# Kernel optimization log

Hardware: AMD Instinct MI355X
Metric: run time of the kernel (lower is better)

The kernel has to match this reference:

```python
import jax, jax.numpy as jnp
import numpy as np

KERNEL_SIZE = 4
SCALE = 0.5


def setup_inputs() -> dict:
    key = jax.random.key(0)
    k1, k2, k3 = jax.random.split(key, 3)
    M, K, N = 16384, 1024, 4096
    x = jax.random.normal(k1, (M, K), dtype=jnp.float32)
    weight = jax.random.normal(k2, (N, K), dtype=jnp.float32)
    bias = jax.random.normal(k3, (N,), dtype=jnp.float32)
    return {"x": x, "weight": weight, "bias": bias}


def reference(x, weight, bias):
    # y = x @ W^T + b : (M, N)
    y = jnp.einsum('mk,nk->mn', x, weight) + bias[None, :]
    M, N = y.shape
    valid_n = (N // KERNEL_SIZE) * KERNEL_SIZE
    # MaxPool1d(kernel_size, stride=kernel_size): (M, N//k, k) -> max over window
    pooled = jnp.max(y[:, :valid_n].reshape(M, valid_n // KERNEL_SIZE, KERNEL_SIZE), axis=-1)
    # sum over pooled features, then scale -> (M,)
    return jnp.sum(pooled, axis=-1) * SCALE
```

## Files before the change

### kernel.cpp

```cpp
#include <hip/hip_runtime.h>
#include <stdint.h>

#define M_DIM 16384
#define K_DIM 1024
#define N_DIM 4096
#define BM 128
#define BN 128
#define LDSP 40

#define TILE_ELEMS (128 * K_DIM)
#define SLAB_ELEMS (128 * 32)
#define NSLAB_X ((M_DIM / 128) * 32)
#define NSLAB_W ((N_DIM / 128) * 32)
#define CROW 20

typedef __bf16 bf16;
typedef __attribute__((ext_vector_type(8))) __bf16 bf16x8;
typedef __attribute__((ext_vector_type(4))) float f32x4;

__device__ __forceinline__ uint32_t pack2_bf16(float a, float b) {
    uint32_t ua = __float_as_uint(a);
    uint32_t ub = __float_as_uint(b);
    ua += 0x7fffu + ((ua >> 16) & 1u);
    ub += 0x7fffu + ((ub >> 16) & 1u);
    return (ua >> 16) | (ub & 0xffff0000u);
}

__global__ __launch_bounds__(256) void convert_pack_kernel(
    const float* __restrict__ x, const float* __restrict__ w,
    bf16* __restrict__ xp, bf16* __restrict__ wp, float* __restrict__ out)
{
    int slab = blockIdx.x;
    const int t = threadIdx.x;
    if (slab < (M_DIM / 256)) out[slab * 256 + t] = 0.f;

    const float* src;
    bf16* dst;
    if (slab < NSLAB_X) { src = x; dst = xp; }
    else                { slab -= NSLAB_X; src = w; dst = wp; }
    const int tile = slab >> 5;
    const int s    = slab & 31;

    __shared__ uint32_t ls[128 * CROW];

    {
        const int r  = t >> 1;
        const int kh = (t & 1) * 16;
        const float4* p = (const float4*)(src + (size_t)(tile * 128 + r) * K_DIM + s * 32 + kh);
        float4 a = p[0], b = p[1], c = p[2], d = p[3];
        uint4* lp = (uint4*)&ls[r * CROW + (t & 1) * 8];
        uint4 v0, v1;
        v0.x = pack2_bf16(a.x, a.y); v0.y = pack2_bf16(a.z, a.w);
        v0.z = pack2_bf16(b.x, b.y); v0.w = pack2_bf16(b.z, b.w);
        v1.x = pack2_bf16(c.x, c.y); v1.y = pack2_bf16(c.z, c.w);
        v1.z = pack2_bf16(d.x, d.y); v1.w = pack2_bf16(d.z, d.w);
        lp[0] = v0; lp[1] = v1;
    }
    __syncthreads();
    uint4* dst4 = (uint4*)(dst + (size_t)tile * TILE_ELEMS + (size_t)s * SLAB_ELEMS);
    #pragma unroll
    for (int p = 0; p < 2; ++p) {
        const int c    = t + p * 256;
        const int lane = c & 63;
        const int rb   = c >> 6;
        const int q    = lane >> 4;
        const int lrow = lane & 15;
        const int r    = rb * 16 + lrow;
        const uint4* lp = (const uint4*)&ls[r * CROW + q * 4];
        dst4[c] = lp[0];
    }
}

__device__ __forceinline__ void load_set(const bf16* base, uint32_t off, bf16x8* f) {
    #pragma unroll
    for (int i = 0; i < 4; ++i) f[i] = *(const bf16x8*)(base + off + i * 512);
}

__device__ __forceinline__ void do_mfma(const bf16x8* af, const bf16x8* bf,
                                        f32x4 acc[4][4]) {
    #pragma unroll
    for (int i = 0; i < 4; ++i)
        #pragma unroll
        for (int j = 0; j < 4; ++j)
            acc[i][j] = __builtin_amdgcn_mfma_f32_16x16x32_bf16(af[i], bf[j], acc[i][j], 0, 0, 0);
}

__global__ __launch_bounds__(256, 4) void gemm_pool_direct_kernel(
    const bf16* __restrict__ xp, const bf16* __restrict__ wp,
    const float* __restrict__ bias, float* __restrict__ out)
{
    const int b     = blockIdx.x;
    const int xcd   = b & 7;
    const int o     = (b >> 3) & 7;
    const int bx    = (b >> 6) & 31;
    const int phase = b >> 11;
    const int by    = phase * 64 + xcd * 8 + o;

    const int lane = threadIdx.x & 63;
    const int wave = threadIdx.x >> 6;
    const int wm = wave >> 1;
    const int wn = wave & 1;
    const int lr = lane & 15;
    const int quad = lane >> 4;

    const bf16* Ab = xp + (size_t)by * TILE_ELEMS;
    const bf16* Bb = wp + (size_t)bx * TILE_ELEMS;
    const uint32_t aoff = (wm * 4) * 512 + lane * 8;
    const uint32_t boff = (wn * 4) * 512 + lane * 8;

    f32x4 acc[4][4] = {};
    bf16x8 aA[4], bA[4], aB[4], bB[4];

    load_set(Ab, aoff, aA);
    load_set(Bb, boff, bA);
    #pragma unroll
    for (int s = 0; s < 32; s += 2) {
        load_set(Ab, aoff + (s + 1) * SLAB_ELEMS, aB);
        load_set(Bb, boff + (s + 1) * SLAB_ELEMS, bB);
        do_mfma(aA, bA, acc);
        if (s + 2 < 32) {
            load_set(Ab, aoff + (s + 2) * SLAB_ELEMS, aA);
            load_set(Bb, boff + (s + 2) * SLAB_ELEMS, bA);
        }
        do_mfma(aB, bB, acc);
    }

    float bv[4];
    #pragma unroll
    for (int j = 0; j < 4; ++j)
        bv[j] = bias[bx * BN + wn * 64 + j * 16 + lr];

    #pragma unroll
    for (int i = 0; i < 4; ++i) {
        float rs[4] = {0.f, 0.f, 0.f, 0.f};
        #pragma unroll
        for (int j = 0; j < 4; ++j) {
            #pragma unroll
            for (int r = 0; r < 4; ++r) {
                float t = acc[i][j][r] + bv[j];
                t = fmaxf(t, __shfl_xor(t, 1, 64));
                t = fmaxf(t, __shfl_xor(t, 2, 64));
                rs[r] += t;
            }
        }
        #pragma unroll
        for (int r = 0; r < 4; ++r) {
            rs[r] += __shfl_xor(rs[r], 4, 64);
            rs[r] += __shfl_xor(rs[r], 8, 64);
        }
        if (lr == 0) {
            const int row = by * BM + wm * 64 + i * 16 + quad * 4;
            #pragma unroll
            for (int r = 0; r < 4; ++r)
                atomicAdd(&out[row + r], rs[r] * 0.5f);
        }
    }
}

__global__ __launch_bounds__(256) void fused_linear_pool_kernel(
    const float* __restrict__ x, const float* __restrict__ wt,
    const float* __restrict__ bias, float* __restrict__ out)
{
    __shared__ uint32_t sA[BM * LDSP / 2];
    __shared__ uint32_t sB[BN * LDSP / 2];

    const int tid = threadIdx.x;
    const int bx = blockIdx.x;
    const int by = blockIdx.y;

    const float* Abase = x  + (size_t)by * BM * K_DIM;
    const float* Bbase = wt + (size_t)bx * BN * K_DIM;

    const int lane = tid & 63;
    const int wave = tid >> 6;
    const int wm = wave >> 1;
    const int wn = wave & 1;
    const int lr = lane & 15;
    const int quad = lane >> 4;

    const int srow  = tid >> 2;
    const int scol  = (tid & 3) * 8;
    const int swidx = (tid & 3) * 4;

    f32x4 acc[4][4] = {};

    for (int kt = 0; kt < K_DIM; kt += 32) {
        #pragma unroll
        for (int p = 0; p < 2; ++p) {
            const int r = srow + p * 64;
            const float4* ga = (const float4*)(Abase + (size_t)r * K_DIM + kt + scol);
            const float4* gb = (const float4*)(Bbase + (size_t)r * K_DIM + kt + scol);
            float4 a0 = ga[0], a1 = ga[1], b0 = gb[0], b1 = gb[1];
            uint4 wa;
            wa.x = pack2_bf16(a0.x, a0.y); wa.y = pack2_bf16(a0.z, a0.w);
            wa.z = pack2_bf16(a1.x, a1.y); wa.w = pack2_bf16(a1.z, a1.w);
            *(uint4*)&sA[r * (LDSP / 2) + swidx] = wa;
            uint4 wbv;
            wbv.x = pack2_bf16(b0.x, b0.y); wbv.y = pack2_bf16(b0.z, b0.w);
            wbv.z = pack2_bf16(b1.x, b1.y); wbv.w = pack2_bf16(b1.z, b1.w);
            *(uint4*)&sB[r * (LDSP / 2) + swidx] = wbv;
        }
        __syncthreads();

        bf16x8 af[4], bfr[4];
        #pragma unroll
        for (int i = 0; i < 4; ++i)
            af[i] = *(const bf16x8*)((const bf16*)sA + (wm * 64 + i * 16 + lr) * LDSP + quad * 8);
        #pragma unroll
        for (int j = 0; j < 4; ++j)
            bfr[j] = *(const bf16x8*)((const bf16*)sB + (wn * 64 + j * 16 + lr) * LDSP + quad * 8);

        #pragma unroll
        for (int i = 0; i < 4; ++i)
            #pragma unroll
            for (int j = 0; j < 4; ++j)
                acc[i][j] = __builtin_amdgcn_mfma_f32_16x16x32_bf16(af[i], bfr[j], acc[i][j], 0, 0, 0);
        __syncthreads();
    }

    float bv[4];
    #pragma unroll
    for (int j = 0; j < 4; ++j)
        bv[j] = bias[bx * BN + wn * 64 + j * 16 + lr];

    #pragma unroll
    for (int i = 0; i < 4; ++i) {
        float rsum[4] = {0.f, 0.f, 0.f, 0.f};
        #pragma unroll
        for (int j = 0; j < 4; ++j) {
            #pragma unroll
            for (int r = 0; r < 4; ++r) {
                float t = acc[i][j][r] + bv[j];
                t = fmaxf(t, __shfl_xor(t, 1, 64));
                t = fmaxf(t, __shfl_xor(t, 2, 64));
                t += __shfl_xor(t, 4, 64);
                t += __shfl_xor(t, 8, 64);
                rsum[r] += t;
            }
        }
        if (lr == 0) {
            const int row = by * BM + wm * 64 + i * 16 + quad * 4;
            #pragma unroll
            for (int r = 0; r < 4; ++r)
                atomicAdd(&out[row + r], rsum[r] * 0.5f);
        }
    }
}

extern "C" void kernel_launch(void* const* d_in, const int* in_sizes, int n_in,
                              void* d_out, int out_size, void* d_ws, size_t ws_size,
                              hipStream_t stream) {
    const float* x  = (const float*)d_in[0];
    const float* wt = (const float*)d_in[1];
    const float* bs = (const float*)d_in[2];
    float* out = (float*)d_out;

    const size_t xe = (size_t)M_DIM * K_DIM;
    const size_t we = (size_t)N_DIM * K_DIM;
    const size_t need = (xe + we) * sizeof(bf16);

    if (ws_size >= need) {
        bf16* xp = (bf16*)d_ws;
        bf16* wp = xp + xe;
        convert_pack_kernel<<<NSLAB_X + NSLAB_W, 256, 0, stream>>>(x, wt, xp, wp, out);
        gemm_pool_direct_kernel<<<(M_DIM / BM) * (N_DIM / BN), 256, 0, stream>>>(xp, wp, bs, out);
    } else {
        hipMemsetAsync(out, 0, (size_t)out_size * sizeof(float), stream);
        dim3 grid(N_DIM / BN, M_DIM / BM);
        fused_linear_pool_kernel<<<grid, 256, 0, stream>>>(x, wt, bs, out);
    }
}
```

Before: 292.3 us.

## Enlarge GEMM block tile to 256 rows with 128x64 per-wave tiles

Each block now covers 256 rows of M instead of 128, and each wave computes a 128x64 output tile using 8x4 MFMA accumulators, which raises the ratio of MFMAs to register-direct global loads. The grid is halved and the block-index swizzle over XCDs is remapped to match. This doubles accumulator and fragment register use, so launch bounds drop to 2 blocks per CU, lowering occupancy and latency hiding.

```diff
diff --git a/kernel.cpp b/kernel.cpp
--- a/kernel.cpp
+++ b/kernel.cpp
@@ -71,30 +71,34 @@
     }
 }
 
-__device__ __forceinline__ void load_set(const bf16* base, uint32_t off, bf16x8* f) {
-    #pragma unroll
-    for (int i = 0; i < 4; ++i) f[i] = *(const bf16x8*)(base + off + i * 512);
-}
-
-__device__ __forceinline__ void do_mfma(const bf16x8* af, const bf16x8* bf,
-                                        f32x4 acc[4][4]) {
-    #pragma unroll
-    for (int i = 0; i < 4; ++i)
+__device__ __forceinline__ void load8(const bf16* base, uint32_t off, bf16x8* f) {
+    #pragma unroll
+    for (int i = 0; i < 8; ++i) f[i] = *(const bf16x8*)(base + off + i * 512);
+}
+__device__ __forceinline__ void load4(const bf16* base, uint32_t off, bf16x8* f) {
+    #pragma unroll
+    for (int j = 0; j < 4; ++j) f[j] = *(const bf16x8*)(base + off + j * 512);
+}
+
+__device__ __forceinline__ void mfma84(const bf16x8* af, const bf16x8* bf,
+                                       f32x4 acc[8][4]) {
+    #pragma unroll
+    for (int i = 0; i < 8; ++i)
         #pragma unroll
         for (int j = 0; j < 4; ++j)
             acc[i][j] = __builtin_amdgcn_mfma_f32_16x16x32_bf16(af[i], bf[j], acc[i][j], 0, 0, 0);
 }
 
-__global__ __launch_bounds__(256, 4) void gemm_pool_direct_kernel(
+__global__ __launch_bounds__(256, 2) void gemm_pool_direct_kernel(
     const bf16* __restrict__ xp, const bf16* __restrict__ wp,
     const float* __restrict__ bias, float* __restrict__ out)
 {
     const int b     = blockIdx.x;
     const int xcd   = b & 7;
-    const int o     = (b >> 3) & 7;
-    const int bx    = (b >> 6) & 31;
-    const int phase = b >> 11;
-    const int by    = phase * 64 + xcd * 8 + o;
+    const int o     = (b >> 3) & 3;
+    const int bx    = (b >> 5) & 31;
+    const int phase = (b >> 10) & 1;
+    const int mt    = phase * 32 + xcd * 4 + o;
 
     const int lane = threadIdx.x & 63;
     const int wave = threadIdx.x >> 6;
@@ -103,26 +107,26 @@
     const int lr = lane & 15;
     const int quad = lane >> 4;
 
-    const bf16* Ab = xp + (size_t)by * TILE_ELEMS;
+    const bf16* Ab = xp + (size_t)(2 * mt + wm) * TILE_ELEMS;
     const bf16* Bb = wp + (size_t)bx * TILE_ELEMS;
-    const uint32_t aoff = (wm * 4) * 512 + lane * 8;
+    const uint32_t aoff = lane * 8;
     const uint32_t boff = (wn * 4) * 512 + lane * 8;
 
-    f32x4 acc[4][4] = {};
-    bf16x8 aA[4], bA[4], aB[4], bB[4];
-
-    load_set(Ab, aoff, aA);
-    load_set(Bb, boff, bA);
+    f32x4 acc[8][4] = {};
+    bf16x8 aA[8], bA[4], aB[8], bB[4];
+
+    load8(Ab, aoff, aA);
+    load4(Bb, boff, bA);
     #pragma unroll
     for (int s = 0; s < 32; s += 2) {
-        load_set(Ab, aoff + (s + 1) * SLAB_ELEMS, aB);
-        load_set(Bb, boff + (s + 1) * SLAB_ELEMS, bB);
-        do_mfma(aA, bA, acc);
+        load8(Ab, aoff + (s + 1) * SLAB_ELEMS, aB);
+        load4(Bb, boff + (s + 1) * SLAB_ELEMS, bB);
+        mfma84(aA, bA, acc);
         if (s + 2 < 32) {
-            load_set(Ab, aoff + (s + 2) * SLAB_ELEMS, aA);
-            load_set(Bb, boff + (s + 2) * SLAB_ELEMS, bA);
-        }
-        do_mfma(aB, bB, acc);
+            load8(Ab, aoff + (s + 2) * SLAB_ELEMS, aA);
+            load4(Bb, boff + (s + 2) * SLAB_ELEMS, bA);
+        }
+        mfma84(aB, bB, acc);
     }
 
     float bv[4];
@@ -130,8 +134,9 @@
     for (int j = 0; j < 4; ++j)
         bv[j] = bias[bx * BN + wn * 64 + j * 16 + lr];
 
-    #pragma unroll
-    for (int i = 0; i < 4; ++i) {
+    const int rowbase = (2 * mt + wm) * 128;
+    #pragma unroll
+    for (int i = 0; i < 8; ++i) {
         float rs[4] = {0.f, 0.f, 0.f, 0.f};
         #pragma unroll
         for (int j = 0; j < 4; ++j) {
@@ -149,7 +154,7 @@
             rs[r] += __shfl_xor(rs[r], 8, 64);
         }
         if (lr == 0) {
-            const int row = by * BM + wm * 64 + i * 16 + quad * 4;
+            const int row = rowbase + i * 16 + quad * 4;
             #pragma unroll
             for (int r = 0; r < 4; ++r)
                 atomicAdd(&out[row + r], rs[r] * 0.5f);
@@ -263,7 +268,7 @@
         bf16* xp = (bf16*)d_ws;
         bf16* wp = xp + xe;
         convert_pack_kernel<<<NSLAB_X + NSLAB_W, 256, 0, stream>>>(x, wt, xp, wp, out);
-        gemm_pool_direct_kernel<<<(M_DIM / BM) * (N_DIM / BN), 256, 0, stream>>>(xp, wp, bs, out);
+        gemm_pool_direct_kernel<<<(M_DIM / 256) * (N_DIM / BN), 256, 0, stream>>>(xp, wp, bs, out);
     } else {
         hipMemsetAsync(out, 0, (size_t)out_size * sizeof(float), stream);
         dim3 grid(N_DIM / BN, M_DIM / BM);
```

Measured after the change: 395.1 us. +35.2%, slower.
